# Optimization experiments

Measured on AMD Instinct MI355X. Metric: run time of the kernel, lower is better.

The kernel has to match this reference:

```python
import jax, jax.numpy as jnp
import numpy as np

N = 10000      # nodes
E = 320000     # edges (avg degree 32)
SI, VI = 256, 32   # node scalar / vector channels
SE, VE = 64, 4     # edge scalar / vector channels
SO, VO = 256, 32   # output channels
IN_S = 2 * SI + SE         # 576 (self_message=True)
IN_V = 2 * VI + VE         # 68
H = max(IN_V, VO)          # 68, GBP hidden vector dim
EPS = 1e-8


def setup_inputs() -> dict:
    key = jax.random.key(0)
    ks = jax.random.split(key, 9)
    node_s = jax.random.normal(ks[0], (N, SI), jnp.float32)
    node_v = jax.random.normal(ks[1], (N, VI, 3), jnp.float32)
    edge_s = jax.random.normal(ks[2], (E, SE), jnp.float32)
    edge_v = jax.random.normal(ks[3], (E, VE, 3), jnp.float32)
    # GBP params (stored as [in, out] so y = x @ W)
    wh = jax.random.normal(ks[4], (IN_V, H), jnp.float32) / np.sqrt(IN_V)
    ws_w = jax.random.normal(ks[5], (IN_S + H, SO), jnp.float32) / np.sqrt(IN_S + H)
    ws_b = jnp.zeros((SO,), jnp.float32)
    wv = jax.random.normal(ks[6], (H, VO), jnp.float32) / np.sqrt(H)
    edge_index = jax.random.randint(ks[7], (2, E), 0, N, jnp.int64)
    return {"node_s": node_s, "node_v": node_v, "edge_s": edge_s,
            "edge_v": edge_v, "wh": wh, "ws_w": ws_w, "ws_b": ws_b,
            "wv": wv, "edge_index": edge_index}


def reference(node_s, node_v, edge_s, edge_v, wh, ws_w, ws_b, wv, edge_index):
    n = node_s.shape[0]
    src, dst = edge_index[0], edge_index[1]
    # gather + tuple_cat((s_j, v_j), edge_attr, (s_i, v_i))
    s_cat = jnp.concatenate([node_s[src], edge_s, node_s[dst]], axis=-1)   # [E, IN_S]
    v_cat = jnp.concatenate([node_v[src], edge_v, node_v[dst]], axis=-2)   # [E, IN_V, 3]
    # GBP message (activations=(None,None), no vector gate)
    v_pre = jnp.swapaxes(v_cat, -1, -2)                # [E, 3, IN_V]
    vh = v_pre @ wh                                    # [E, 3, H]
    vn = jnp.sqrt(jnp.maximum(jnp.sum(vh * vh, axis=-2), EPS))  # _norm_no_nan, [E, H]
    s_msg = jnp.concatenate([s_cat, vn], axis=-1) @ ws_w + ws_b  # [E, SO]
    v_msg = jnp.swapaxes(vh @ wv, -1, -2)              # [E, VO, 3]
    # scatter-mean to target nodes
    agg_s = jax.ops.segment_sum(s_msg, dst, num_segments=n)       # [N, SO]
    agg_v = jax.ops.segment_sum(v_msg, dst, num_segments=n)       # [N, VO, 3]
    cnt = jax.ops.segment_sum(jnp.ones((s_msg.shape[0],), s_msg.dtype), dst,
                              num_segments=n)
    cnt = jnp.maximum(cnt, 1.0)
    out_s = agg_s / cnt[:, None]
    out_v = agg_v / cnt[:, None, None]
    # _merge(s, V): flatten vector channels and append to scalars
    return jnp.concatenate([out_s, out_v.reshape(n, 3 * VO)], axis=-1)  # [N, SO+3*VO]
```

## Files before the change

kernel.cpp:

```cpp
#include <hip/hip_runtime.h>
#include <hip/hip_bf16.h>

#define N_NODES 10000
#define E_TOT   320000

typedef __attribute__((ext_vector_type(8))) short short8;
typedef __attribute__((ext_vector_type(4))) short s16x4;
typedef __attribute__((ext_vector_type(4))) float f32x4;

#define HIST_OFF    0u
#define FILL_OFF    40000u
#define ZERO_BYTES  80000u
#define ROWPTR_OFF  80000u
#define PERM_OFF    120064u
#define PSRC_OFF    1400064u
#define CN_OFF      2680064u
#define QARR_OFF    13560064u
#define QV_OFF      17720064u
#define WHV4_OFF    19640064u
#define WBIG_OFF    19640576u
#define NSBF_OFF    19984640u
#define ANSB_OFF    25104640u
#define EAB_OFF     30224640u
#define AP_OFF      33424640u
#define AEV_OFF     41584640u
#define FLAGS_OFF   42064640u
#define NODES_OFF   120064u

union BfS { __hip_bfloat16 h; short s; };
__device__ __forceinline__ short f2bf(float x) { BfS u; u.h = __float2bfloat16(x); return u.s; }
__device__ __forceinline__ float bf(short x) { BfS u; u.s = x; return __bfloat162float(u.h); }
__device__ __forceinline__ float bflo(unsigned u) { return __uint_as_float(u << 16); }
__device__ __forceinline__ float bfhi(unsigned u) { return __uint_as_float(u & 0xffff0000u); }
__device__ __forceinline__ float ldin(const void* p, int f32m, long i) {
  return f32m ? ((const float*)p)[i] : __bfloat162float(((const __hip_bfloat16*)p)[i]);
}
__device__ __forceinline__ int get_ei(const void* p, int i64m, long i) {
  return i64m ? (int)(((const long long*)p)[i]) : ((const int*)p)[i];
}

__global__ __launch_bounds__(256) void detect_kernel(
    const unsigned short* __restrict__ ns_u16,
    const int* __restrict__ ei_i32, int* __restrict__ flags)
{
  __shared__ int cf, ci;
  if (threadIdx.x == 0) { cf = 0; ci = 0; }
  __syncthreads();
  int c1 = 0;
  for (int i = threadIdx.x; i < 8192; i += 256) {
    unsigned e = (ns_u16[2 * i] >> 7) & 0xFF;
    if (e < 100 || e > 140) c1++;
  }
  int c2 = 0;
  for (int i = threadIdx.x; i < 4096; i += 256)
    if (ei_i32[2 * i + 1] != 0) c2++;
  atomicAdd(&cf, c1); atomicAdd(&ci, c2);
  __syncthreads();
  if (threadIdx.x == 0) {
    flags[0] = (cf > 512) ? 1 : 0;
    flags[1] = (ci < 100) ? 1 : 0;
  }
}

__global__ __launch_bounds__(256) void hist_kernel(
    const void* __restrict__ edge_index, const int* __restrict__ flags,
    int* __restrict__ hist)
{
  const int i64m = flags[1];
  int e = blockIdx.x * 256 + threadIdx.x;
  int dst = get_ei(edge_index, i64m, (long)E_TOT + e);
  atomicAdd(&hist[dst], 1);
}

__global__ __launch_bounds__(256) void scan_kernel(
    const int* __restrict__ hist, int* __restrict__ rowptr)
{
  __shared__ int part[256];
  int tid = threadIdx.x;
  int base = tid * 40;
  int s = 0;
  for (int i = 0; i < 40; ++i) { int idx = base + i; if (idx < N_NODES) s += hist[idx]; }
  part[tid] = s;
  __syncthreads();
  for (int off = 1; off < 256; off <<= 1) {
    int v = (tid >= off) ? part[tid - off] : 0;
    __syncthreads();
    part[tid] += v;
    __syncthreads();
  }
  int run = (tid > 0) ? part[tid - 1] : 0;
  for (int i = 0; i < 40; ++i) {
    int idx = base + i;
    if (idx < N_NODES) { rowptr[idx] = run; run += hist[idx]; }
  }
  if (tid == 255) rowptr[N_NODES] = run;
}

__global__ __launch_bounds__(256) void permute_kernel(
    const void* __restrict__ edge_index, const int* __restrict__ flags,
    const int* __restrict__ rowptr, int* __restrict__ fill,
    int* __restrict__ perm, int* __restrict__ psrc)
{
  const int i64m = flags[1];
  int e = blockIdx.x * 256 + threadIdx.x;
  int dst = get_ei(edge_index, i64m, (long)E_TOT + e);
  int src = get_ei(edge_index, i64m, e);
  int pos = rowptr[dst] + atomicAdd(&fill[dst], 1);
  perm[pos] = e; psrc[pos] = src;
}

__global__ __launch_bounds__(256) void prep_kernel(
    const void* __restrict__ ws_w, const void* __restrict__ wh,
    const void* __restrict__ wv, const int* __restrict__ flags,
    short* __restrict__ Wbig, float* __restrict__ whv4)
{
  const int f32m = flags[0];
  int b = blockIdx.x, tid = threadIdx.x;
  if (b < 672) {
    int flat = b * 256 + tid;
    int o = flat / 672, k = flat % 672;
    short v = 0;
    if (k < 320)      v = f2bf(ldin(ws_w, f32m, (long)k * 256 + o));
    else if (k < 388) v = f2bf(ldin(ws_w, f32m, (long)(576 + k - 320) * 256 + o));
    else if (k >= 416) v = f2bf(ldin(ws_w, f32m, (long)(k - 96) * 256 + o));
    Wbig[flat] = v;
  } else if (tid < 128) {
    int q = tid / 32, c = tid % 32;
    float acc = 0.f;
    for (int h = 0; h < 68; ++h)
      acc += ldin(wh, f32m, (32 + q) * 68 + h) * ldin(wv, f32m, h * 32 + c);
    whv4[tid] = acc;
  }
}

__global__ __launch_bounds__(256) void node_pre(
    const void* __restrict__ node_v, const void* __restrict__ wh,
    const void* __restrict__ wv, const void* __restrict__ node_s,
    const int* __restrict__ flags,
    short* __restrict__ CN, short* __restrict__ QARR,
    short* __restrict__ QV, short* __restrict__ ns_bf)
{
  const int f32m = flags[0];
  int n0 = blockIdx.x * 4, tid = threadIdx.x;
  __shared__ float whs[68 * 68];
  __shared__ float wvs[68 * 32];
  __shared__ float nv[4][96];
  __shared__ float pq[4][408];
  for (int i = tid; i < 4624; i += 256) whs[i] = ldin(wh, f32m, i);
  for (int i = tid; i < 2176; i += 256) wvs[i] = ldin(wv, f32m, i);
  for (int i = tid; i < 4 * 96; i += 256) nv[i / 96][i % 96] = ldin(node_v, f32m, (long)n0 * 96 + i);
  for (int i = tid; i < 1024; i += 256)
    ns_bf[(long)n0 * 256 + i] = f2bf(ldin(node_s, f32m, (long)n0 * 256 + i));
  __syncthreads();
  for (int o = tid; o < 4 * 408; o += 256) {
    int i = o / 408, r0 = o % 408;
    int part = r0 / 204, r = r0 % 204, d = r / 68, h = r % 68;
    int cbase = part ? 36 : 0;
    float acc = 0.f;
#pragma unroll
    for (int c = 0; c < 32; ++c)
      acc += nv[i][c * 3 + d] * whs[(cbase + c) * 68 + h];
    pq[i][r0] = acc;
  }
  __syncthreads();
  for (int o = tid; o < 4 * 544; o += 256) {
    int i = o / 544, k = o % 544;
    short v = 0;
    if (k < 512) {
      int l = k >> 3, j = k & 7;
      if (j < 4)      v = f2bf(ldin(node_s, f32m, (long)(n0 + i) * 256 + l * 4 + j));
      else if (j < 7) v = f2bf(pq[i][(j - 4) * 68 + l]);
    } else if (k < 528) {
      int idx = k - 512, jj = idx >> 2, d = idx & 3;
      if (d < 3) v = f2bf(pq[i][d * 68 + 64 + jj]);
    }
    CN[(long)(n0 + i) * 544 + k] = v;
  }
  for (int o = tid; o < 4 * 208; o += 256) {
    int i = o / 208, k = o % 208;
    QARR[(long)(n0 + i) * 208 + k] = (k < 204) ? f2bf(pq[i][204 + k]) : (short)0;
  }
  for (int o = tid; o < 4 * 96; o += 256) {
    int i = o / 96, r = o % 96, d = r / 32, c = r % 32;
    float acc = 0.f;
    for (int h = 0; h < 68; ++h)
      acc += pq[i][204 + d * 68 + h] * wvs[h * 32 + c];
    QV[(long)(n0 + i) * 96 + r] = f2bf(acc);
  }
}

struct EdgeLds {
  float ansL[4][256];
  float apL[4][204];
  float avnL[4][132];
  float aesL[4][64];
  float aevL[4][12];
};

template <int F32M>
__device__ __forceinline__ void edge_body(
    const void* __restrict__ edge_v, const void* __restrict__ edge_s,
    const void* __restrict__ wh,
    const int* __restrict__ rowptr, const int* __restrict__ perm,
    const int* __restrict__ psrc, const short* __restrict__ CN,
    const short* __restrict__ QARR,
    short* __restrict__ ANSb, short* __restrict__ EAb,
    float* __restrict__ AP, float* __restrict__ AEV, EdgeLds* lds)
{
  const int tid = threadIdx.x;
  const int lane = tid & 63, w = tid >> 6;
  const int n = blockIdx.x;
  const int beg = rowptr[n], deg = rowptr[n + 1] - beg;
  const bool has2 = (lane < 4);
  const int h2 = 64 + lane;
  const float w4a0 = ldin(wh, F32M, 32 * 68 + lane);
  const float w4a1 = ldin(wh, F32M, 33 * 68 + lane);
  const float w4a2 = ldin(wh, F32M, 34 * 68 + lane);
  const float w4a3 = ldin(wh, F32M, 35 * 68 + lane);
  const float w4b0 = has2 ? ldin(wh, F32M, 32 * 68 + h2) : 0.f;
  const float w4b1 = has2 ? ldin(wh, F32M, 33 * 68 + h2) : 0.f;
  const float w4b2 = has2 ? ldin(wh, F32M, 34 * 68 + h2) : 0.f;
  const float w4b3 = has2 ? ldin(wh, F32M, 35 * 68 + h2) : 0.f;
  const short* qp = QARR + (long)n * 208;
  const float qa0 = bf(qp[0 * 68 + lane]);
  const float qa1 = bf(qp[1 * 68 + lane]);
  const float qa2 = bf(qp[2 * 68 + lane]);
  const float qb0 = has2 ? bf(qp[0 * 68 + h2]) : 0.f;
  const float qb1 = has2 ? bf(qp[1 * 68 + h2]) : 0.f;
  const float qb2 = has2 ? bf(qp[2 * 68 + h2]) : 0.f;
  float an0 = 0.f, an1 = 0.f, an2 = 0.f, an3 = 0.f;
  float ap0 = 0.f, ap1 = 0.f, ap2 = 0.f;
  float bq0 = 0.f, bq1 = 0.f, bq2 = 0.f;
  float avna = 0.f, avnb = 0.f, aes = 0.f, aev = 0.f;
  int e = w;
  int sv = 0, eid = 0;
  if (e < deg) { sv = psrc[beg + e]; eid = perm[beg + e]; }
  while (e < deg) {
    int en = e + 4, svn = 0, eidn = 0;
    if (en < deg) { svn = psrc[beg + en]; eidn = perm[beg + en]; }
    const int sv_s  = __builtin_amdgcn_readfirstlane(sv);
    const int eid_s = __builtin_amdgcn_readfirstlane(eid);
    float ev0, ev1, ev2, ev3, ev4, ev5, ev6, ev7, ev8, ev9, evA, evB;
    if (F32M) {
      const float* evp = (const float*)edge_v + (long)eid_s * 12;
      ev0 = evp[0]; ev1 = evp[1]; ev2 = evp[2]; ev3 = evp[3];
      ev4 = evp[4]; ev5 = evp[5]; ev6 = evp[6]; ev7 = evp[7];
      ev8 = evp[8]; ev9 = evp[9]; evA = evp[10]; evB = evp[11];
    } else {
      const unsigned* evp = (const unsigned*)((const short*)edge_v + (long)eid_s * 12);
      unsigned u0 = evp[0], u1 = evp[1], u2 = evp[2];
      unsigned u3 = evp[3], u4 = evp[4], u5 = evp[5];
      ev0 = bflo(u0); ev1 = bfhi(u0); ev2 = bflo(u1); ev3 = bfhi(u1);
      ev4 = bflo(u2); ev5 = bfhi(u2); ev6 = bflo(u3); ev7 = bfhi(u3);
      ev8 = bflo(u4); ev9 = bfhi(u4); evA = bflo(u5); evB = bfhi(u5);
    }
    const short* cs = CN + (long)sv_s * 544;
    short8 cv = *(const short8*)(cs + lane * 8);
    an0 += bf(cv[0]); an1 += bf(cv[1]); an2 += bf(cv[2]); an3 += bf(cv[3]);
    const float pa0 = bf(cv[4]), pa1 = bf(cv[5]), pa2 = bf(cv[6]);
    aes += ldin(edge_s, F32M, (long)eid_s * 64 + lane);
    if (lane < 12) aev += ldin(edge_v, F32M, (long)eid_s * 12 + lane);
    float v0 = pa0 + qa0 + ev0 * w4a0 + ev3 * w4a1 + ev6 * w4a2 + ev9 * w4a3;
    float v1 = pa1 + qa1 + ev1 * w4a0 + ev4 * w4a1 + ev7 * w4a2 + evA * w4a3;
    float v2 = pa2 + qa2 + ev2 * w4a0 + ev5 * w4a1 + ev8 * w4a2 + evB * w4a3;
    avna += sqrtf(fmaxf(v0 * v0 + v1 * v1 + v2 * v2, 1e-8f));
    ap0 += pa0; ap1 += pa1; ap2 += pa2;
    if (has2) {
      s16x4 p2 = *(const s16x4*)(cs + 512 + lane * 4);
      const float pb0 = bf(p2.x), pb1 = bf(p2.y), pb2 = bf(p2.z);
      float u0 = pb0 + qb0 + ev0 * w4b0 + ev3 * w4b1 + ev6 * w4b2 + ev9 * w4b3;
      float u1 = pb1 + qb1 + ev1 * w4b0 + ev4 * w4b1 + ev7 * w4b2 + evA * w4b3;
      float u2 = pb2 + qb2 + ev2 * w4b0 + ev5 * w4b1 + ev8 * w4b2 + evB * w4b3;
      avnb += sqrtf(fmaxf(u0 * u0 + u1 * u1 + u2 * u2, 1e-8f));
      bq0 += pb0; bq1 += pb1; bq2 += pb2;
    }
    e = en; sv = svn; eid = eidn;
  }
  lds->ansL[w][lane * 4 + 0] = an0; lds->ansL[w][lane * 4 + 1] = an1;
  lds->ansL[w][lane * 4 + 2] = an2; lds->ansL[w][lane * 4 + 3] = an3;
  lds->apL[w][lane * 3 + 0] = ap0; lds->apL[w][lane * 3 + 1] = ap1;
  lds->apL[w][lane * 3 + 2] = ap2;
  if (has2) {
    lds->apL[w][192 + lane * 3 + 0] = bq0;
    lds->apL[w][192 + lane * 3 + 1] = bq1;
    lds->apL[w][192 + lane * 3 + 2] = bq2;
  }
  lds->avnL[w][lane] = avna;
  if (has2) lds->avnL[w][64 + lane] = avnb;
  lds->aesL[w][lane] = aes;
  if (lane < 12) lds->aevL[w][lane] = aev;
  __syncthreads();
  const float inv = 1.f / fmaxf((float)deg, 1.f);
  {
    float s = lds->ansL[0][tid] + lds->ansL[1][tid] + lds->ansL[2][tid] + lds->ansL[3][tid];
    ANSb[(long)n * 256 + tid] = f2bf(s * inv);
  }
  if (tid < 204) {
    float s = lds->apL[0][tid] + lds->apL[1][tid] + lds->apL[2][tid] + lds->apL[3][tid];
    AP[(long)n * 204 + tid] = s;
  } else if (tid < 216) {
    int c = tid - 204;
    float s = lds->aevL[0][c] + lds->aevL[1][c] + lds->aevL[2][c] + lds->aevL[3][c];
    AEV[(long)n * 12 + c] = s;
  }
  if (tid < 64) {
    float s = lds->aesL[0][tid] + lds->aesL[1][tid] + lds->aesL[2][tid] + lds->aesL[3][tid];
    EAb[(long)n * 160 + tid] = f2bf(s * inv);
  } else if (tid < 132) {
    int c = tid - 64;
    float s = lds->avnL[0][c] + lds->avnL[1][c] + lds->avnL[2][c] + lds->avnL[3][c];
    EAb[(long)n * 160 + 64 + c] = f2bf(s * inv);
  } else if (tid < 160) {
    EAb[(long)n * 160 + tid] = 0;
  }
}

__global__ __launch_bounds__(256) void edge_block(
    const void* __restrict__ edge_v, const void* __restrict__ edge_s,
    const void* __restrict__ wh, const int* __restrict__ flags,
    const int* __restrict__ rowptr, const int* __restrict__ perm,
    const int* __restrict__ psrc, const short* __restrict__ CN,
    const short* __restrict__ QARR,
    short* __restrict__ ANSb, short* __restrict__ EAb,
    float* __restrict__ AP, float* __restrict__ AEV)
{
  __shared__ EdgeLds lds;
  if (flags[0])
    edge_body<1>(edge_v, edge_s, wh, rowptr, perm, psrc, CN, QARR,
                 ANSb, EAb, AP, AEV, &lds);
  else
    edge_body<0>(edge_v, edge_s, wh, rowptr, perm, psrc, CN, QARR,
                 ANSb, EAb, AP, AEV, &lds);
}

__global__ __launch_bounds__(256) void node_gemm(
    const short* __restrict__ ANSb, const short* __restrict__ EAb,
    const short* __restrict__ nsb, const short* __restrict__ Wbig,
    float* __restrict__ NodeS)
{
  __shared__ __align__(16) short Xs[64 * 40];
  __shared__ __align__(16) short Ws[256 * 40];
  const int tid = threadIdx.x;
  const int n0 = blockIdx.x * 64;
  const int lane = tid & 63, wave = tid >> 6;
  const int frow = lane & 15, fk = (lane >> 4) * 8, q = lane >> 4;
  f32x4 acc[4][4];
#pragma unroll
  for (int ri = 0; ri < 4; ++ri)
#pragma unroll
    for (int ci = 0; ci < 4; ++ci)
      acc[ri][ci] = (f32x4){0.f, 0.f, 0.f, 0.f};
  const int se = tid >> 2, sq = tid & 3;
  const int rn = min(n0 + se, N_NODES - 1);
  for (int s = 0; s < 21; ++s) {
    short8 xv;
    if (s < 8)       xv = *(const short8*)&ANSb[(long)rn * 256 + s * 32 + sq * 8];
    else if (s < 13) xv = *(const short8*)&EAb[(long)rn * 160 + (s - 8) * 32 + sq * 8];
    else             xv = *(const short8*)&nsb[(long)rn * 256 + (s - 13) * 32 + sq * 8];
    *(short8*)&Xs[se * 40 + sq * 8] = xv;
#pragma unroll
    for (int it = 0; it < 4; ++it) {
      int flat = it * 256 + tid;
      int nn = flat >> 2, qq = flat & 3;
      *(short8*)&Ws[nn * 40 + qq * 8] = *(const short8*)&Wbig[nn * 672 + s * 32 + qq * 8];
    }
    __syncthreads();
    short8 a[4];
#pragma unroll
    for (int ri = 0; ri < 4; ++ri)
      a[ri] = *(const short8*)&Xs[(ri * 16 + frow) * 40 + fk];
#pragma unroll
    for (int ci = 0; ci < 4; ++ci) {
      int nn = wave * 64 + ci * 16 + frow;
      short8 b = *(const short8*)&Ws[nn * 40 + fk];
#pragma unroll
      for (int ri = 0; ri < 4; ++ri)
        acc[ri][ci] = __builtin_amdgcn_mfma_f32_16x16x32_bf16(a[ri], b, acc[ri][ci], 0, 0, 0);
    }
    __syncthreads();
  }
#pragma unroll
  for (int ri = 0; ri < 4; ++ri)
#pragma unroll
    for (int rr = 0; rr < 4; ++rr) {
      int row = n0 + ri * 16 + q * 4 + rr;
      if (row < N_NODES) {
#pragma unroll
        for (int ci = 0; ci < 4; ++ci) {
          int col = wave * 64 + ci * 16 + (lane & 15);
          NodeS[(long)row * 256 + col] = acc[ri][ci][rr];
        }
      }
    }
}

__global__ __launch_bounds__(256) void final_fuse(
    const float* __restrict__ NodeS, const float* __restrict__ AP,
    const float* __restrict__ AEV, const void* __restrict__ wv,
    const float* __restrict__ whv4, const int* __restrict__ rowptr,
    const short* __restrict__ QV, const void* __restrict__ ws_b,
    const int* __restrict__ flags, void* __restrict__ out)
{
  const int f32m = flags[0];
  int n0 = blockIdx.x * 4, tid = threadIdx.x;
  __shared__ float wvs[68 * 32];
  __shared__ float wh4s[128];
  __shared__ float APs[4][204];
  __shared__ float AEVs[4][12];
  __shared__ float aggL[4][96];
  for (int i = tid; i < 2176; i += 256) wvs[i] = ldin(wv, f32m, i);
  if (tid < 128) wh4s[tid] = whv4[tid];
  for (int i = tid; i < 816; i += 256) APs[i / 204][i % 204] = AP[(long)n0 * 204 + i];
  if (tid < 48) AEVs[tid / 12][tid % 12] = AEV[(long)n0 * 12 + tid];
  __syncthreads();
  for (int o = tid; o < 384; o += 256) {
    int i = o / 96, r = o % 96, c = r / 3, d = r % 3;
    float acc = AEVs[i][d] * wh4s[c] + AEVs[i][3 + d] * wh4s[32 + c]
              + AEVs[i][6 + d] * wh4s[64 + c] + AEVs[i][9 + d] * wh4s[96 + c];
    for (int h = 0; h < 68; ++h)
      acc += APs[i][h * 3 + d] * wvs[h * 32 + c];
    aggL[i][r] = acc;
  }
  __syncthreads();
  for (int o = tid; o < 1408; o += 256) {
    int i = o / 352, j = o % 352;
    int n = n0 + i;
    int deg = rowptr[n + 1] - rowptr[n];
    float v;
    if (j < 256) {
      v = (deg > 0) ? (NodeS[(long)n * 256 + j] + ldin(ws_b, f32m, j)) : 0.f;
    } else {
      int m = j - 256, ch = m / 3, d = m % 3;
      float inv = 1.f / fmaxf((float)deg, 1.f);
      v = aggL[i][m] * inv;
      if (deg > 0) v += bf(QV[(long)n * 96 + d * 32 + ch]);
    }
    long flat = (long)n * 352 + j;
    if (f32m) ((float*)out)[flat] = v;
    else      ((__hip_bfloat16*)out)[flat] = __float2bfloat16(v);
  }
}

extern "C" void kernel_launch(void* const* d_in, const int* in_sizes, int n_in,
                              void* d_out, int out_size, void* d_ws, size_t ws_size,
                              hipStream_t stream) {
  const void* node_s = d_in[0];
  const void* node_v = d_in[1];
  const void* edge_s = d_in[2];
  const void* edge_v = d_in[3];
  const void* wh     = d_in[4];
  const void* ws_w   = d_in[5];
  const void* ws_b   = d_in[6];
  const void* wv     = d_in[7];
  const void* edge_index = d_in[8];

  char* ws = (char*)d_ws;
  int*   hist  = (int*)(ws + HIST_OFF);
  int*   fill  = (int*)(ws + FILL_OFF);
  int*   rowptr= (int*)(ws + ROWPTR_OFF);
  int*   perm  = (int*)(ws + PERM_OFF);
  int*   psrc  = (int*)(ws + PSRC_OFF);
  short* CN    = (short*)(ws + CN_OFF);
  short* QARR  = (short*)(ws + QARR_OFF);
  short* QV    = (short*)(ws + QV_OFF);
  float* whv4  = (float*)(ws + WHV4_OFF);
  short* Wbig  = (short*)(ws + WBIG_OFF);
  short* ns_bf = (short*)(ws + NSBF_OFF);
  short* ANSb  = (short*)(ws + ANSB_OFF);
  short* EAb   = (short*)(ws + EAB_OFF);
  float* AP    = (float*)(ws + AP_OFF);
  float* AEV   = (float*)(ws + AEV_OFF);
  float* NodeS = (float*)(ws + NODES_OFF);
  int*   flags = (int*)(ws + FLAGS_OFF);

  hipMemsetAsync(d_ws, 0, ZERO_BYTES, stream);
  detect_kernel<<<1, 256, 0, stream>>>((const unsigned short*)node_s,
                                       (const int*)edge_index, flags);
  hist_kernel<<<1250, 256, 0, stream>>>(edge_index, flags, hist);
  scan_kernel<<<1, 256, 0, stream>>>(hist, rowptr);
  permute_kernel<<<1250, 256, 0, stream>>>(edge_index, flags, rowptr, fill,
                                           perm, psrc);
  prep_kernel<<<673, 256, 0, stream>>>(ws_w, wh, wv, flags, Wbig, whv4);
  node_pre<<<2500, 256, 0, stream>>>(node_v, wh, wv, node_s, flags,
                                     CN, QARR, QV, ns_bf);
  edge_block<<<10000, 256, 0, stream>>>(edge_v, edge_s, wh, flags, rowptr,
                                        perm, psrc, CN, QARR,
                                        ANSb, EAb, AP, AEV);
  node_gemm<<<157, 256, 0, stream>>>(ANSb, EAb, ns_bf, Wbig, NodeS);
  final_fuse<<<2500, 256, 0, stream>>>(NodeS, AP, AEV, wv, whv4, rowptr,
                                       QV, ws_b, flags, d_out);
}
```

Baseline: 446.6 us.

## Fuse preprocessing kernels and unroll edge loop by two edges

```diff
diff --git a/kernel.cpp b/kernel.cpp
--- a/kernel.cpp
+++ b/kernel.cpp
@@ -39,47 +39,49 @@
   return i64m ? (int)(((const long long*)p)[i]) : ((const int*)p)[i];
 }
 
-__global__ __launch_bounds__(256) void detect_kernel(
-    const unsigned short* __restrict__ ns_u16,
-    const int* __restrict__ ei_i32, int* __restrict__ flags)
-{
-  __shared__ int cf, ci;
-  if (threadIdx.x == 0) { cf = 0; ci = 0; }
-  __syncthreads();
-  int c1 = 0;
-  for (int i = threadIdx.x; i < 8192; i += 256) {
-    unsigned e = (ns_u16[2 * i] >> 7) & 0xFF;
-    if (e < 100 || e > 140) c1++;
-  }
-  int c2 = 0;
-  for (int i = threadIdx.x; i < 4096; i += 256)
-    if (ei_i32[2 * i + 1] != 0) c2++;
-  atomicAdd(&cf, c1); atomicAdd(&ci, c2);
-  __syncthreads();
-  if (threadIdx.x == 0) {
-    flags[0] = (cf > 512) ? 1 : 0;
-    flags[1] = (ci < 100) ? 1 : 0;
-  }
-}
-
-__global__ __launch_bounds__(256) void hist_kernel(
-    const void* __restrict__ edge_index, const int* __restrict__ flags,
-    int* __restrict__ hist)
-{
-  const int i64m = flags[1];
-  int e = blockIdx.x * 256 + threadIdx.x;
+__global__ __launch_bounds__(256) void hist_det(
+    const void* __restrict__ edge_index, const unsigned short* __restrict__ ns_u16,
+    int* __restrict__ hist, int* __restrict__ flags)
+{
+  const int tid = threadIdx.x;
+  const int* ei = (const int*)edge_index;
+  int nz = (ei[2 * tid + 1] != 0) ? 1 : 0;
+  unsigned long long m = __ballot(nz);
+  __shared__ int cnt4[4];
+  if ((tid & 63) == 0) cnt4[tid >> 6] = __popcll(m);
+  __syncthreads();
+  const int i64m = (cnt4[0] + cnt4[1] + cnt4[2] + cnt4[3]) < 16 ? 1 : 0;
+  int e = blockIdx.x * 256 + tid;
   int dst = get_ei(edge_index, i64m, (long)E_TOT + e);
   atomicAdd(&hist[dst], 1);
-}
-
-__global__ __launch_bounds__(256) void scan_kernel(
-    const int* __restrict__ hist, int* __restrict__ rowptr)
-{
+  if (blockIdx.x == 0) {
+    __shared__ int cf;
+    if (tid == 0) cf = 0;
+    __syncthreads();
+    int c1 = 0;
+    for (int i = tid; i < 8192; i += 256) {
+      unsigned ex = (ns_u16[2 * i] >> 7) & 0xFF;
+      if (ex < 100 || ex > 140) c1++;
+    }
+    atomicAdd(&cf, c1);
+    __syncthreads();
+    if (tid == 0) { flags[0] = (cf > 512) ? 1 : 0; flags[1] = i64m; }
+  }
+}
+
+__global__ __launch_bounds__(256) void scanperm(
+    const void* __restrict__ edge_index, const int* __restrict__ flags,
+    const int* __restrict__ hist, int* __restrict__ rowptr,
+    int* __restrict__ fill, int* __restrict__ perm, int* __restrict__ psrc)
+{
+  __shared__ int rp[N_NODES];
   __shared__ int part[256];
-  int tid = threadIdx.x;
-  int base = tid * 40;
+  const int tid = threadIdx.x;
+  for (int i = tid; i < N_NODES; i += 256) rp[i] = hist[i];
+  __syncthreads();
+  const int base = tid * 40;
   int s = 0;
-  for (int i = 0; i < 40; ++i) { int idx = base + i; if (idx < N_NODES) s += hist[idx]; }
+  for (int i = 0; i < 40; ++i) { int idx = base + i; if (idx < N_NODES) s += rp[idx]; }
   part[tid] = s;
   __syncthreads();
   for (int off = 1; off < 256; off <<= 1) {
@@ -91,61 +93,55 @@
   int run = (tid > 0) ? part[tid - 1] : 0;
   for (int i = 0; i < 40; ++i) {
     int idx = base + i;
-    if (idx < N_NODES) { rowptr[idx] = run; run += hist[idx]; }
-  }
-  if (tid == 255) rowptr[N_NODES] = run;
-}
-
-__global__ __launch_bounds__(256) void permute_kernel(
-    const void* __restrict__ edge_index, const int* __restrict__ flags,
-    const int* __restrict__ rowptr, int* __restrict__ fill,
-    int* __restrict__ perm, int* __restrict__ psrc)
-{
+    if (idx < N_NODES) { int h = rp[idx]; rp[idx] = run; run += h; }
+  }
+  __syncthreads();
+  if (blockIdx.x == 0) {
+    for (int i = tid; i < N_NODES; i += 256) rowptr[i] = rp[i];
+    if (tid == 0) rowptr[N_NODES] = part[255];
+  }
   const int i64m = flags[1];
-  int e = blockIdx.x * 256 + threadIdx.x;
+  int e = blockIdx.x * 256 + tid;
   int dst = get_ei(edge_index, i64m, (long)E_TOT + e);
   int src = get_ei(edge_index, i64m, e);
-  int pos = rowptr[dst] + atomicAdd(&fill[dst], 1);
+  int pos = rp[dst] + atomicAdd(&fill[dst], 1);
   perm[pos] = e; psrc[pos] = src;
 }
 
-__global__ __launch_bounds__(256) void prep_kernel(
-    const void* __restrict__ ws_w, const void* __restrict__ wh,
-    const void* __restrict__ wv, const int* __restrict__ flags,
-    short* __restrict__ Wbig, float* __restrict__ whv4)
-{
-  const int f32m = flags[0];
-  int b = blockIdx.x, tid = threadIdx.x;
-  if (b < 672) {
-    int flat = b * 256 + tid;
-    int o = flat / 672, k = flat % 672;
-    short v = 0;
-    if (k < 320)      v = f2bf(ldin(ws_w, f32m, (long)k * 256 + o));
-    else if (k < 388) v = f2bf(ldin(ws_w, f32m, (long)(576 + k - 320) * 256 + o));
-    else if (k >= 416) v = f2bf(ldin(ws_w, f32m, (long)(k - 96) * 256 + o));
-    Wbig[flat] = v;
-  } else if (tid < 128) {
-    int q = tid / 32, c = tid % 32;
-    float acc = 0.f;
-    for (int h = 0; h < 68; ++h)
-      acc += ldin(wh, f32m, (32 + q) * 68 + h) * ldin(wv, f32m, h * 32 + c);
-    whv4[tid] = acc;
-  }
-}
-
-__global__ __launch_bounds__(256) void node_pre(
+__global__ __launch_bounds__(256) void node_pre_prep(
     const void* __restrict__ node_v, const void* __restrict__ wh,
     const void* __restrict__ wv, const void* __restrict__ node_s,
-    const int* __restrict__ flags,
+    const void* __restrict__ ws_w, const int* __restrict__ flags,
     short* __restrict__ CN, short* __restrict__ QARR,
-    short* __restrict__ QV, short* __restrict__ ns_bf)
+    short* __restrict__ QV, short* __restrict__ ns_bf,
+    short* __restrict__ Wbig, float* __restrict__ whv4)
 {
   const int f32m = flags[0];
-  int n0 = blockIdx.x * 4, tid = threadIdx.x;
+  const int b = blockIdx.x, tid = threadIdx.x;
   __shared__ float whs[68 * 68];
   __shared__ float wvs[68 * 32];
   __shared__ float nv[4][96];
   __shared__ float pq[4][408];
+  if (b >= 2500) {
+    int pb = b - 2500;
+    if (pb < 672) {
+      int flat = pb * 256 + tid;
+      int o = flat / 672, k = flat % 672;
+      short v = 0;
+      if (k < 320)      v = f2bf(ldin(ws_w, f32m, (long)k * 256 + o));
+      else if (k < 388) v = f2bf(ldin(ws_w, f32m, (long)(576 + k - 320) * 256 + o));
+      else if (k >= 416) v = f2bf(ldin(ws_w, f32m, (long)(k - 96) * 256 + o));
+      Wbig[flat] = v;
+    } else if (tid < 128) {
+      int q = tid / 32, c = tid % 32;
+      float acc = 0.f;
+      for (int h = 0; h < 68; ++h)
+        acc += ldin(wh, f32m, (32 + q) * 68 + h) * ldin(wv, f32m, h * 32 + c);
+      whv4[tid] = acc;
+    }
+    return;
+  }
+  int n0 = b * 4;
   for (int i = tid; i < 4624; i += 256) whs[i] = ldin(wh, f32m, i);
   for (int i = tid; i < 2176; i += 256) wvs[i] = ldin(wv, f32m, i);
   for (int i = tid; i < 4 * 96; i += 256) nv[i / 96][i % 96] = ldin(node_v, f32m, (long)n0 * 96 + i);
@@ -233,48 +229,92 @@
   float bq0 = 0.f, bq1 = 0.f, bq2 = 0.f;
   float avna = 0.f, avnb = 0.f, aes = 0.f, aev = 0.f;
   int e = w;
-  int sv = 0, eid = 0;
-  if (e < deg) { sv = psrc[beg + e]; eid = perm[beg + e]; }
+  int sv0 = 0, id0 = 0, sv1 = 0, id1 = 0;
+  if (e < deg)     { sv0 = psrc[beg + e];     id0 = perm[beg + e]; }
+  if (e + 4 < deg) { sv1 = psrc[beg + e + 4]; id1 = perm[beg + e + 4]; }
   while (e < deg) {
-    int en = e + 4, svn = 0, eidn = 0;
-    if (en < deg) { svn = psrc[beg + en]; eidn = perm[beg + en]; }
-    const int sv_s  = __builtin_amdgcn_readfirstlane(sv);
-    const int eid_s = __builtin_amdgcn_readfirstlane(eid);
-    float ev0, ev1, ev2, ev3, ev4, ev5, ev6, ev7, ev8, ev9, evA, evB;
+    const bool p1 = (e + 4 < deg);
+    const int en = e + 8;
+    int nsv0 = 0, nid0 = 0, nsv1 = 0, nid1 = 0;
+    if (en < deg)     { nsv0 = psrc[beg + en];     nid0 = perm[beg + en]; }
+    if (en + 4 < deg) { nsv1 = psrc[beg + en + 4]; nid1 = perm[beg + en + 4]; }
+    const int s0 = __builtin_amdgcn_readfirstlane(sv0);
+    const int d0 = __builtin_amdgcn_readfirstlane(id0);
+    const int s1 = __builtin_amdgcn_readfirstlane(sv1);
+    const int d1 = __builtin_amdgcn_readfirstlane(id1);
+    const short* cs0 = CN + (long)s0 * 544;
+    const short* cs1 = CN + (long)s1 * 544;
+    short8 cva = *(const short8*)(cs0 + lane * 8);
+    short8 cvb = *(const short8*)(cs1 + lane * 8);
+    float esa = ldin(edge_s, F32M, (long)d0 * 64 + lane);
+    float esb = ldin(edge_s, F32M, (long)d1 * 64 + lane);
+    float eva_l = 0.f, evb_l = 0.f;
+    if (lane < 12) {
+      eva_l = ldin(edge_v, F32M, (long)d0 * 12 + lane);
+      evb_l = ldin(edge_v, F32M, (long)d1 * 12 + lane);
+    }
+    float a0, a1, a2, a3, a4, a5, a6, a7, a8, a9, aA, aB;
+    float b0, b1, b2, b3, b4, b5, b6, b7, b8, b9, bA, bB;
     if (F32M) {
-      const float* evp = (const float*)edge_v + (long)eid_s * 12;
-      ev0 = evp[0]; ev1 = evp[1]; ev2 = evp[2]; ev3 = evp[3];
-      ev4 = evp[4]; ev5 = evp[5]; ev6 = evp[6]; ev7 = evp[7];
-      ev8 = evp[8]; ev9 = evp[9]; evA = evp[10]; evB = evp[11];
+      const float* evp0 = (const float*)edge_v + (long)d0 * 12;
+      const float* evp1 = (const float*)edge_v + (long)d1 * 12;
+      a0 = evp0[0]; a1 = evp0[1]; a2 = evp0[2]; a3 = evp0[3];
+      a4 = evp0[4]; a5 = evp0[5]; a6 = evp0[6]; a7 = evp0[7];
+      a8 = evp0[8]; a9 = evp0[9]; aA = evp0[10]; aB = evp0[11];
+      b0 = evp1[0]; b1 = evp1[1]; b2 = evp1[2]; b3 = evp1[3];
+      b4 = evp1[4]; b5 = evp1[5]; b6 = evp1[6]; b7 = evp1[7];
+      b8 = evp1[8]; b9 = evp1[9]; bA = evp1[10]; bB = evp1[11];
     } else {
-      const unsigned* evp = (const unsigned*)((const short*)edge_v + (long)eid_s * 12);
-      unsigned u0 = evp[0], u1 = evp[1], u2 = evp[2];
-      unsigned u3 = evp[3], u4 = evp[4], u5 = evp[5];
-      ev0 = bflo(u0); ev1 = bfhi(u0); ev2 = bflo(u1); ev3 = bfhi(u1);
-      ev4 = bflo(u2); ev5 = bfhi(u2); ev6 = bflo(u3); ev7 = bfhi(u3);
-      ev8 = bflo(u4); ev9 = bfhi(u4); evA = bflo(u5); evB = bfhi(u5);
-    }
-    const short* cs = CN + (long)sv_s * 544;
-    short8 cv = *(const short8*)(cs + lane * 8);
-    an0 += bf(cv[0]); an1 += bf(cv[1]); an2 += bf(cv[2]); an3 += bf(cv[3]);
-    const float pa0 = bf(cv[4]), pa1 = bf(cv[5]), pa2 = bf(cv[6]);
-    aes += ldin(edge_s, F32M, (long)eid_s * 64 + lane);
-    if (lane < 12) aev += ldin(edge_v, F32M, (long)eid_s * 12 + lane);
-    float v0 = pa0 + qa0 + ev0 * w4a0 + ev3 * w4a1 + ev6 * w4a2 + ev9 * w4a3;
-    float v1 = pa1 + qa1 + ev1 * w4a0 + ev4 * w4a1 + ev7 * w4a2 + evA * w4a3;
-    float v2 = pa2 + qa2 + ev2 * w4a0 + ev5 * w4a1 + ev8 * w4a2 + evB * w4a3;
-    avna += sqrtf(fmaxf(v0 * v0 + v1 * v1 + v2 * v2, 1e-8f));
-    ap0 += pa0; ap1 += pa1; ap2 += pa2;
-    if (has2) {
-      s16x4 p2 = *(const s16x4*)(cs + 512 + lane * 4);
-      const float pb0 = bf(p2.x), pb1 = bf(p2.y), pb2 = bf(p2.z);
-      float u0 = pb0 + qb0 + ev0 * w4b0 + ev3 * w4b1 + ev6 * w4b2 + ev9 * w4b3;
-      float u1 = pb1 + qb1 + ev1 * w4b0 + ev4 * w4b1 + ev7 * w4b2 + evA * w4b3;
-      float u2 = pb2 + qb2 + ev2 * w4b0 + ev5 * w4b1 + ev8 * w4b2 + evB * w4b3;
-      avnb += sqrtf(fmaxf(u0 * u0 + u1 * u1 + u2 * u2, 1e-8f));
-      bq0 += pb0; bq1 += pb1; bq2 += pb2;
-    }
-    e = en; sv = svn; eid = eidn;
+      const unsigned* e0p = (const unsigned*)((const short*)edge_v + (long)d0 * 12);
+      const unsigned* e1p = (const unsigned*)((const short*)edge_v + (long)d1 * 12);
+      unsigned u0 = e0p[0], u1 = e0p[1], u2 = e0p[2], u3 = e0p[3], u4 = e0p[4], u5 = e0p[5];
+      unsigned v0 = e1p[0], v1 = e1p[1], v2 = e1p[2], v3 = e1p[3], v4 = e1p[4], v5 = e1p[5];
+      a0 = bflo(u0); a1 = bfhi(u0); a2 = bflo(u1); a3 = bfhi(u1);
+      a4 = bflo(u2); a5 = bfhi(u2); a6 = bflo(u3); a7 = bfhi(u3);
+      a8 = bflo(u4); a9 = bfhi(u4); aA = bflo(u5); aB = bfhi(u5);
+      b0 = bflo(v0); b1 = bfhi(v0); b2 = bflo(v1); b3 = bfhi(v1);
+      b4 = bflo(v2); b5 = bfhi(v2); b6 = bflo(v3); b7 = bfhi(v3);
+      b8 = bflo(v4); b9 = bfhi(v4); bA = bflo(v5); bB = bfhi(v5);
+    }
+    {
+      an0 += bf(cva[0]); an1 += bf(cva[1]); an2 += bf(cva[2]); an3 += bf(cva[3]);
+      const float pa0 = bf(cva[4]), pa1 = bf(cva[5]), pa2 = bf(cva[6]);
+      aes += esa; aev += eva_l;
+      float v0 = pa0 + qa0 + a0 * w4a0 + a3 * w4a1 + a6 * w4a2 + a9 * w4a3;
+      float v1 = pa1 + qa1 + a1 * w4a0 + a4 * w4a1 + a7 * w4a2 + aA * w4a3;
+      float v2 = pa2 + qa2 + a2 * w4a0 + a5 * w4a1 + a8 * w4a2 + aB * w4a3;
+      avna += sqrtf(fmaxf(v0 * v0 + v1 * v1 + v2 * v2, 1e-8f));
+      ap0 += pa0; ap1 += pa1; ap2 += pa2;
+      if (has2) {
+        s16x4 p2 = *(const s16x4*)(cs0 + 512 + lane * 4);
+        const float pb0 = bf(p2.x), pb1 = bf(p2.y), pb2 = bf(p2.z);
+        float u0 = pb0 + qb0 + a0 * w4b0 + a3 * w4b1 + a6 * w4b2 + a9 * w4b3;
+        float u1 = pb1 + qb1 + a1 * w4b0 + a4 * w4b1 + a7 * w4b2 + aA * w4b3;
+        float u2 = pb2 + qb2 + a2 * w4b0 + a5 * w4b1 + a8 * w4b2 + aB * w4b3;
+        avnb += sqrtf(fmaxf(u0 * u0 + u1 * u1 + u2 * u2, 1e-8f));
+        bq0 += pb0; bq1 += pb1; bq2 += pb2;
+      }
+    }
+    if (p1) {
+      an0 += bf(cvb[0]); an1 += bf(cvb[1]); an2 += bf(cvb[2]); an3 += bf(cvb[3]);
+      const float pa0 = bf(cvb[4]), pa1 = bf(cvb[5]), pa2 = bf(cvb[6]);
+      aes += esb; aev += evb_l;
+      float v0 = pa0 + qa0 + b0 * w4a0 + b3 * w4a1 + b6 * w4a2 + b9 * w4a3;
+      float v1 = pa1 + qa1 + b1 * w4a0 + b4 * w4a1 + b7 * w4a2 + bA * w4a3;
+      float v2 = pa2 + qa2 + b2 * w4a0 + b5 * w4a1 + b8 * w4a2 + bB * w4a3;
+      avna += sqrtf(fmaxf(v0 * v0 + v1 * v1 + v2 * v2, 1e-8f));
+      ap0 += pa0; ap1 += pa1; ap2 += pa2;
+      if (has2) {
+        s16x4 p2 = *(const s16x4*)(cs1 + 512 + lane * 4);
+        const float pb0 = bf(p2.x), pb1 = bf(p2.y), pb2 = bf(p2.z);
+        float u0 = pb0 + qb0 + b0 * w4b0 + b3 * w4b1 + b6 * w4b2 + b9 * w4b3;
+        float u1 = pb1 + qb1 + b1 * w4b0 + b4 * w4b1 + b7 * w4b2 + bA * w4b3;
+        float u2 = pb2 + qb2 + b2 * w4b0 + b5 * w4b1 + b8 * w4b2 + bB * w4b3;
+        avnb += sqrtf(fmaxf(u0 * u0 + u1 * u1 + u2 * u2, 1e-8f));
+        bq0 += pb0; bq1 += pb1; bq2 += pb2;
+      }
+    }
+    e = en; sv0 = nsv0; id0 = nid0; sv1 = nsv1; id1 = nid1;
   }
   lds->ansL[w][lane * 4 + 0] = an0; lds->ansL[w][lane * 4 + 1] = an1;
   lds->ansL[w][lane * 4 + 2] = an2; lds->ansL[w][lane * 4 + 3] = an3;
@@ -474,15 +514,12 @@
   int*   flags = (int*)(ws + FLAGS_OFF);
 
   hipMemsetAsync(d_ws, 0, ZERO_BYTES, stream);
-  detect_kernel<<<1, 256, 0, stream>>>((const unsigned short*)node_s,
-                                       (const int*)edge_index, flags);
-  hist_kernel<<<1250, 256, 0, stream>>>(edge_index, flags, hist);
-  scan_kernel<<<1, 256, 0, stream>>>(hist, rowptr);
-  permute_kernel<<<1250, 256, 0, stream>>>(edge_index, flags, rowptr, fill,
-                                           perm, psrc);
-  prep_kernel<<<673, 256, 0, stream>>>(ws_w, wh, wv, flags, Wbig, whv4);
-  node_pre<<<2500, 256, 0, stream>>>(node_v, wh, wv, node_s, flags,
-                                     CN, QARR, QV, ns_bf);
+  hist_det<<<1250, 256, 0, stream>>>(edge_index, (const unsigned short*)node_s,
+                                     hist, flags);
+  scanperm<<<1250, 256, 0, stream>>>(edge_index, flags, hist, rowptr, fill,
+                                     perm, psrc);
+  node_pre_prep<<<3173, 256, 0, stream>>>(node_v, wh, wv, node_s, ws_w, flags,
+                                          CN, QARR, QV, ns_bf, Wbig, whv4);
   edge_block<<<10000, 256, 0, stream>>>(edge_v, edge_s, wh, flags, rowptr,
                                         perm, psrc, CN, QARR,
                                         ANSb, EAb, AP, AEV);
```

New measurement: 434.1 us. 2.8% less time.
